# Kernel tuning notes

Hardware: AMD Instinct MI355X
Metric: run time of the kernel (lower is better)

## Reference

```python
import jax, jax.numpy as jnp
import numpy as np

N, DIM = 8192, 128

def setup_inputs() -> dict:
    key = jax.random.key(0)
    ks = jax.random.split(key, 9)
    s = 1.0 / np.sqrt(DIM)
    return {
        "x": jax.random.normal(ks[0], (N, DIM), dtype=jnp.float32),
        "Wq": jax.random.uniform(ks[1], (DIM, DIM), jnp.float32, -s, s),
        "bq": jax.random.uniform(ks[2], (DIM,), jnp.float32, -s, s),
        "Wk": jax.random.uniform(ks[3], (DIM, DIM), jnp.float32, -s, s),
        "bk": jax.random.uniform(ks[4], (DIM,), jnp.float32, -s, s),
        "Wv": jax.random.uniform(ks[5], (DIM, DIM), jnp.float32, -s, s),
        "bv": jax.random.uniform(ks[6], (DIM,), jnp.float32, -s, s),
        "Wo": jax.random.uniform(ks[7], (DIM, DIM), jnp.float32, -s, s),
        "bo": jax.random.uniform(ks[8], (DIM,), jnp.float32, -s, s),
    }

def reference(x, Wq, bq, Wk, bk, Wv, bv, Wo, bo):
    # nn.Linear: y = x @ W.T + b
    Q = x @ Wq.T + bq                      # [N, d]
    K = x @ Wk.T + bk                      # [N, d]
    V = x @ Wv.T + bv                      # [N, d]
    scale = 1.0 / jnp.sqrt(jnp.asarray(x.shape[-1], x.dtype))
    scores = (Q @ K.T) * scale             # [N, N] — matches original O(n^2) math
    attn = jax.nn.softmax(scores, axis=-1)
    out = attn @ V                         # [N, d]
    return out @ Wo.T + bo
```

## Files before the change

kernel.cpp:

```cpp
#include <hip/hip_runtime.h>
#include <math.h>


typedef __bf16 bf16x8 __attribute__((ext_vector_type(8)));
typedef float f32x4 __attribute__((ext_vector_type(4)));
typedef float f32x16 __attribute__((ext_vector_type(16)));
typedef unsigned int u32x4 __attribute__((ext_vector_type(4)));
typedef unsigned int u32x2 __attribute__((ext_vector_type(2)));
typedef unsigned short us16;

#define NTOK 8192
#define CHUNKS 8

static constexpr float SCALE_L2E = 0.08838834764831845f * 1.4426950408889634f;

__device__ __forceinline__ unsigned f2bf_u(float x) {
    unsigned u = __builtin_bit_cast(unsigned, x);
    return (u + 0x7FFFu + ((u >> 16) & 1u)) >> 16;
}

__device__ __forceinline__ unsigned pk_bf16(float x, float y) {
    unsigned a = __builtin_bit_cast(unsigned, x) + 0x8000u;
    unsigned b = __builtin_bit_cast(unsigned, y) + 0x8000u;
#if __has_builtin(__builtin_amdgcn_perm)
    return __builtin_amdgcn_perm(b, a, 0x07060302u);
#else
    return (a >> 16) | (b & 0xFFFF0000u);
#endif
}

__device__ __forceinline__ unsigned cvtpk_bf16(float x, float y) {
    unsigned r;
    asm("v_cvt_pk_bf16_f32 %0, %1, %2" : "=v"(r) : "v"(x), "v"(y));
    return r;
}

__device__ __forceinline__ void plswap(unsigned& a, unsigned& b) {
    asm("v_permlane32_swap_b32 %0, %1" : "+v"(a), "+v"(b));
}

__device__ __forceinline__ void pl16swap(unsigned& a, unsigned& b) {
    asm("v_permlane16_swap_b32 %0, %1" : "+v"(a), "+v"(b));
}

__device__ __forceinline__ float fexp2(float x) {
#if __has_builtin(__builtin_amdgcn_exp2f)
    return __builtin_amdgcn_exp2f(x);
#else
    return exp2f(x);
#endif
}

__device__ __forceinline__ bf16x8 ld_frag(const us16* p) {
    u32x4 u = *reinterpret_cast<const u32x4*>(p);
    return __builtin_bit_cast(bf16x8, u);
}

__device__ __forceinline__ bf16x8 cvt_frag(const float* p) {
    f32x4 a = *reinterpret_cast<const f32x4*>(p);
    f32x4 b = *reinterpret_cast<const f32x4*>(p + 4);
    u32x4 o;
    o[0] = f2bf_u(a[0]) | (f2bf_u(a[1]) << 16);
    o[1] = f2bf_u(a[2]) | (f2bf_u(a[3]) << 16);
    o[2] = f2bf_u(b[0]) | (f2bf_u(b[1]) << 16);
    o[3] = f2bf_u(b[2]) | (f2bf_u(b[3]) << 16);
    return __builtin_bit_cast(bf16x8, o);
}

__global__ __launch_bounds__(256) void proj_qkv(
    const float* __restrict__ x,
    const float* __restrict__ wq, const float* __restrict__ bq,
    const float* __restrict__ wk, const float* __restrict__ bk,
    const float* __restrict__ wv, const float* __restrict__ bv,
    us16* __restrict__ Qb, us16* __restrict__ Kb, us16* __restrict__ Vt)
{
    __shared__ us16 ldsT[4][16 * 136];

    int z = blockIdx.x >> 7;
    int tile = blockIdx.x & 127;
    const float* W = z == 0 ? wq : z == 1 ? wk : wv;
    const float* bias = z == 0 ? bq : z == 1 ? bk : bv;
    float osc = z == 0 ? SCALE_L2E : 1.0f;

    int w = threadIdx.x >> 6, lane = threadIdx.x & 63;
    int quad = lane >> 4, l15 = lane & 15;
    int rbase = tile * 64 + w * 16;

    bf16x8 af[4];
#pragma unroll
    for (int ks = 0; ks < 4; ++ks)
        af[ks] = cvt_frag(x + (rbase + l15) * 128 + ks * 32 + quad * 8);

    f32x4 acc[8];
#pragma unroll
    for (int nt = 0; nt < 8; ++nt) acc[nt] = f32x4{0.f, 0.f, 0.f, 0.f};

#pragma unroll
    for (int nt = 0; nt < 8; ++nt) {
#pragma unroll
        for (int ks = 0; ks < 4; ++ks) {
            bf16x8 bf = cvt_frag(W + (nt * 16 + l15) * 128 + ks * 32 + quad * 8);
            acc[nt] = __builtin_amdgcn_mfma_f32_16x16x32_bf16(af[ks], bf, acc[nt], 0, 0, 0);
        }
    }

    if (z < 2) {
        us16* T = &ldsT[w][0];
        us16* Out = z == 0 ? Qb : Kb;
#pragma unroll
        for (int nt = 0; nt < 8; ++nt) {
            float bb = bias[nt * 16 + l15];
#pragma unroll
            for (int r = 0; r < 4; ++r)
                T[(quad * 4 + r) * 136 + nt * 16 + l15] =
                    (us16)f2bf_u((acc[nt][r] + bb) * osc);
        }
        asm volatile("s_waitcnt lgkmcnt(0)" ::: "memory");
        __builtin_amdgcn_sched_barrier(0);
        int row = lane >> 2, seg = lane & 3;
        const us16* src = T + row * 136 + seg * 32;
        us16* dst = Out + (rbase + row) * 128 + seg * 32;
#pragma unroll
        for (int c = 0; c < 4; ++c)
            *reinterpret_cast<u32x4*>(dst + c * 8) =
                *reinterpret_cast<const u32x4*>(src + c * 8);
    } else {
#pragma unroll
        for (int nt = 0; nt < 8; ++nt) {
            float bb = bias[nt * 16 + l15];
            int d = nt * 16 + l15, r0 = rbase + quad * 4;
            u32x2 pk;
            pk[0] = f2bf_u(acc[nt][0] + bb) | (f2bf_u(acc[nt][1] + bb) << 16);
            pk[1] = f2bf_u(acc[nt][2] + bb) | (f2bf_u(acc[nt][3] + bb) << 16);
            *reinterpret_cast<u32x2*>(Vt + d * NTOK + r0) = pk;
        }
    }
}

__global__ __launch_bounds__(256, 2) void attn(
    const us16* __restrict__ Qb, const us16* __restrict__ Kb,
    const us16* __restrict__ Vt,
    float* __restrict__ Opart, float* __restrict__ Lpart)
{
    __shared__ us16 ldsK[2][64 * 136];
    __shared__ us16 ldsV[2][128 * 72];

    int qtile = blockIdx.x >> 3, chunk = blockIdx.x & 7;
    int tid = threadIdx.x, w = tid >> 6, lane = tid & 63;
    int quad = lane >> 4, l15 = lane & 15;
    int qb0 = qtile * 128 + w * 32;
    int k0 = chunk * 1024;

    bf16x8 qf[2][4];
#pragma unroll
    for (int mt = 0; mt < 2; ++mt)
#pragma unroll
        for (int ks = 0; ks < 4; ++ks)
            qf[mt][ks] = ld_frag(Qb + (qb0 + mt * 16 + l15) * 128 + ks * 32 + quad * 8);

    f32x4 o[2][8];
#pragma unroll
    for (int mt = 0; mt < 2; ++mt)
#pragma unroll
        for (int dt = 0; dt < 8; ++dt) o[mt][dt] = f32x4{0.f, 0.f, 0.f, 0.f};

    f32x4 lacc[2];
    lacc[0] = f32x4{0.f, 0.f, 0.f, 0.f};
    lacc[1] = f32x4{0.f, 0.f, 0.f, 0.f};

    u32x4 onesu;
    onesu[0] = onesu[1] = onesu[2] = onesu[3] = 0x3F803F80u;
    bf16x8 ones = __builtin_bit_cast(bf16x8, onesu);

#pragma unroll
    for (int c = 0; c < 4; ++c) {
        int idx = tid + c * 256, r = idx >> 4, cc = idx & 15;
        *reinterpret_cast<u32x4*>(&ldsK[0][0] + r * 136 + cc * 8) =
            *reinterpret_cast<const u32x4*>(Kb + (k0 + r) * 128 + cc * 8);
    }
#pragma unroll
    for (int c = 0; c < 4; ++c) {
        int idx = tid + c * 256, r = idx >> 3, cc = idx & 7;
        *reinterpret_cast<u32x4*>(&ldsV[0][0] + r * 72 + cc * 8) =
            *reinterpret_cast<const u32x4*>(Vt + (size_t)r * NTOK + k0 + cc * 8);
    }
    __syncthreads();

    for (int it = 0; it < 16; ++it) {
        int cur = it & 1;
        const us16* K_ = &ldsK[cur][0];
        const us16* V_ = &ldsV[cur][0];

        u32x4 kreg[4], vreg[4];
        if (it < 15) {
            int kk = k0 + (it + 1) * 64;
#pragma unroll
            for (int c = 0; c < 4; ++c) {
                int idx = tid + c * 256, r = idx >> 4, cc = idx & 15;
                kreg[c] = *reinterpret_cast<const u32x4*>(Kb + (kk + r) * 128 + cc * 8);
            }
#pragma unroll
            for (int c = 0; c < 4; ++c) {
                int idx = tid + c * 256, r = idx >> 3, cc = idx & 7;
                vreg[c] = *reinterpret_cast<const u32x4*>(Vt + (size_t)r * NTOK + kk + cc * 8);
            }
            __builtin_amdgcn_sched_barrier(0);
        }

        f32x4 s[2][4];
#pragma unroll
        for (int mt = 0; mt < 2; ++mt)
#pragma unroll
            for (int nt = 0; nt < 4; ++nt) s[mt][nt] = f32x4{0.f, 0.f, 0.f, 0.f};

        __builtin_amdgcn_s_setprio(1);
#pragma unroll
        for (int nt = 0; nt < 4; ++nt) {
#pragma unroll
            for (int ks = 0; ks < 4; ++ks) {
                bf16x8 kf = ld_frag(K_ + (nt * 16 + l15) * 136 + ks * 32 + quad * 8);
                s[0][nt] = __builtin_amdgcn_mfma_f32_16x16x32_bf16(kf, qf[0][ks], s[0][nt], 0, 0, 0);
                s[1][nt] = __builtin_amdgcn_mfma_f32_16x16x32_bf16(kf, qf[1][ks], s[1][nt], 0, 0, 0);
            }
        }
        __builtin_amdgcn_s_setprio(0);

        bf16x8 afP[2][2];
#pragma unroll
        for (int mt = 0; mt < 2; ++mt) {
            unsigned W[4][2];
#pragma unroll
            for (int nt = 0; nt < 4; ++nt) {
                float p0 = fexp2(s[mt][nt][0]);
                float p1 = fexp2(s[mt][nt][1]);
                float p2 = fexp2(s[mt][nt][2]);
                float p3 = fexp2(s[mt][nt][3]);
                W[nt][0] = cvtpk_bf16(p0, p1);
                W[nt][1] = cvtpk_bf16(p2, p3);
            }
#pragma unroll
            for (int k2 = 0; k2 < 2; ++k2) {
                u32x4 f;
                {
                    unsigned X = W[2 * k2][0], Y = W[2 * k2 + 1][0];
                    plswap(X, Y); pl16swap(X, Y);
                    f[0] = X; f[2] = Y;
                }
                {
                    unsigned X = W[2 * k2][1], Y = W[2 * k2 + 1][1];
                    plswap(X, Y); pl16swap(X, Y);
                    f[1] = X; f[3] = Y;
                }
                afP[mt][k2] = __builtin_bit_cast(bf16x8, f);
            }
        }

        lacc[0] = __builtin_amdgcn_mfma_f32_16x16x32_bf16(afP[0][0], ones, lacc[0], 0, 0, 0);
        lacc[0] = __builtin_amdgcn_mfma_f32_16x16x32_bf16(afP[0][1], ones, lacc[0], 0, 0, 0);
        lacc[1] = __builtin_amdgcn_mfma_f32_16x16x32_bf16(afP[1][0], ones, lacc[1], 0, 0, 0);
        lacc[1] = __builtin_amdgcn_mfma_f32_16x16x32_bf16(afP[1][1], ones, lacc[1], 0, 0, 0);

        __builtin_amdgcn_s_setprio(1);
#pragma unroll
        for (int dt = 0; dt < 8; ++dt) {
#pragma unroll
            for (int k2 = 0; k2 < 2; ++k2) {
                bf16x8 bv = ld_frag(V_ + (dt * 16 + l15) * 72 + k2 * 32 + quad * 8);
                o[0][dt] = __builtin_amdgcn_mfma_f32_16x16x32_bf16(afP[0][k2], bv, o[0][dt], 0, 0, 0);
                o[1][dt] = __builtin_amdgcn_mfma_f32_16x16x32_bf16(afP[1][k2], bv, o[1][dt], 0, 0, 0);
            }
        }
        __builtin_amdgcn_s_setprio(0);

        if (it < 15) {
            __builtin_amdgcn_sched_barrier(0);
#pragma unroll
            for (int c = 0; c < 4; ++c) {
                int idx = tid + c * 256, r = idx >> 4, cc = idx & 15;
                *reinterpret_cast<u32x4*>(&ldsK[cur ^ 1][0] + r * 136 + cc * 8) = kreg[c];
            }
#pragma unroll
            for (int c = 0; c < 4; ++c) {
                int idx = tid + c * 256, r = idx >> 3, cc = idx & 7;
                *reinterpret_cast<u32x4*>(&ldsV[cur ^ 1][0] + r * 72 + cc * 8) = vreg[c];
            }
        }
        __syncthreads();
    }

#pragma unroll
    for (int mt = 0; mt < 2; ++mt)
#pragma unroll
        for (int dt = 0; dt < 8; ++dt)
#pragma unroll
            for (int r = 0; r < 4; ++r) {
                int row = qb0 + mt * 16 + quad * 4 + r;
                Opart[(size_t)(chunk * NTOK + row) * 128 + dt * 16 + l15] = o[mt][dt][r];
            }
    if (l15 == 0) {
#pragma unroll
        for (int mt = 0; mt < 2; ++mt)
#pragma unroll
            for (int r = 0; r < 4; ++r) {
                int row = qb0 + mt * 16 + quad * 4 + r;
                Lpart[chunk * NTOK + row] = lacc[mt][r];
            }
    }
}

__global__ __launch_bounds__(256) void combine_proj(
    const float* __restrict__ Opart, const float* __restrict__ Lpart,
    const float* __restrict__ Wo, const float* __restrict__ bo,
    float* __restrict__ out)
{
    __shared__ us16 ldsO[32 * 136];
    __shared__ float ldsL[32];

    int tile = blockIdx.x, t = threadIdx.x;
    int r0 = tile * 32;

    if (t < 32) {
        float L = 0.f;
#pragma unroll
        for (int c = 0; c < CHUNKS; ++c) L += Lpart[c * NTOK + r0 + t];
        ldsL[t] = 1.0f / L;
    }

    f32x4 acc[4];
#pragma unroll
    for (int j = 0; j < 4; ++j) acc[j] = f32x4{0.f, 0.f, 0.f, 0.f};

#pragma unroll
    for (int c = 0; c < CHUNKS; ++c) {
        const float* src = Opart + (size_t)(c * NTOK + r0) * 128;
#pragma unroll
        for (int j = 0; j < 4; ++j) {
            f32x4 v = *reinterpret_cast<const f32x4*>(src + j * 1024 + t * 4);
            acc[j] += v;
        }
    }
    __syncthreads();

#pragma unroll
    for (int j = 0; j < 4; ++j) {
        int flat = j * 1024 + t * 4;
        int row = flat >> 7, col = flat & 127;
        float sc = ldsL[row];
        u32x2 wv;
        wv[0] = pk_bf16(acc[j][0] * sc, acc[j][1] * sc);
        wv[1] = pk_bf16(acc[j][2] * sc, acc[j][3] * sc);
        *reinterpret_cast<u32x2*>(ldsO + row * 136 + col) = wv;
    }
    __syncthreads();

    int w = t >> 6, lane = t & 63;
    int l31 = lane & 31, hi = lane >> 5;

    bf16x8 af[8];
#pragma unroll
    for (int ks = 0; ks < 8; ++ks)
        af[ks] = ld_frag(ldsO + l31 * 136 + ks * 16 + hi * 8);

    f32x16 acc2;
#pragma unroll
    for (int r = 0; r < 16; ++r) acc2[r] = 0.f;

#pragma unroll
    for (int ks = 0; ks < 8; ++ks) {
        bf16x8 bfw = cvt_frag(Wo + (w * 32 + l31) * 128 + ks * 16 + hi * 8);
        acc2 = __builtin_amdgcn_mfma_f32_32x32x16_bf16(af[ks], bfw, acc2, 0, 0, 0);
    }

    float bb = bo[w * 32 + l31];
#pragma unroll
    for (int r = 0; r < 16; ++r) {
        int m = (r & 3) + 8 * (r >> 2) + 4 * hi;
        out[(size_t)(r0 + m) * 128 + w * 32 + l31] = acc2[r] + bb;
    }
}

extern "C" void kernel_launch(void* const* d_in, const int* in_sizes, int n_in,
                              void* d_out, int out_size, void* d_ws, size_t ws_size,
                              hipStream_t stream)
{
    const float* x  = (const float*)d_in[0];
    const float* Wq = (const float*)d_in[1];
    const float* bq = (const float*)d_in[2];
    const float* Wk = (const float*)d_in[3];
    const float* bk = (const float*)d_in[4];
    const float* Wv = (const float*)d_in[5];
    const float* bv = (const float*)d_in[6];
    const float* Wo = (const float*)d_in[7];
    const float* bo = (const float*)d_in[8];

    char* ws = (char*)d_ws;
    const size_t MB = 1024 * 1024;
    us16* Qb  = (us16*)(ws + 0 * MB);
    us16* Kb  = (us16*)(ws + 2 * MB);
    us16* Vt  = (us16*)(ws + 4 * MB);
    float* Lp = (float*)(ws + 6 * MB);
    float* Op = (float*)(ws + 7 * MB);

    proj_qkv<<<384, 256, 0, stream>>>(x, Wq, bq, Wk, bk, Wv, bv, Qb, Kb, Vt);
    attn<<<512, 256, 0, stream>>>(Qb, Kb, Vt, Op, Lp);
    combine_proj<<<256, 256, 0, stream>>>(Op, Lp, Wo, bo, (float*)d_out);
}
```

Baseline: 139.6 us.

## Double attention block to 512 threads with 128-key tiles and shared K/V

The attention kernel now runs 8 waves per block covering 256 query rows, and 256 blocks instead of 512. Each loop iteration stages 128 keys instead of 64, processed in two halves, so half as many barriers and a larger K/V reuse across waves per LDS load. LDS grows to about 136 KB per block, which forces one block per CU and may reduce latency hiding; the grid also shrinks to 256 blocks, matching the CU count.

```diff
diff --git a/kernel.cpp b/kernel.cpp
--- a/kernel.cpp
+++ b/kernel.cpp
@@ -11,6 +11,8 @@
 
 #define NTOK 8192
 #define CHUNKS 8
+#define KT2 (128 * 136)
+#define VT2 (128 * 136)
 
 static constexpr float SCALE_L2E = 0.08838834764831845f * 1.4426950408889634f;
 
@@ -137,19 +139,22 @@
     }
 }
 
-__global__ __launch_bounds__(256, 2) void attn(
+__global__ __launch_bounds__(512, 1) void attn(
     const us16* __restrict__ Qb, const us16* __restrict__ Kb,
     const us16* __restrict__ Vt,
     float* __restrict__ Opart, float* __restrict__ Lpart)
 {
-    __shared__ us16 ldsK[2][64 * 136];
-    __shared__ us16 ldsV[2][128 * 72];
-
-    int qtile = blockIdx.x >> 3, chunk = blockIdx.x & 7;
+    __shared__ us16 smem[2 * KT2 + 2 * VT2];
+
+    int bid = blockIdx.x;
+    int qtile = bid >> 3, chunk = bid & 7;
     int tid = threadIdx.x, w = tid >> 6, lane = tid & 63;
     int quad = lane >> 4, l15 = lane & 15;
-    int qb0 = qtile * 128 + w * 32;
+    int qb0 = qtile * 256 + w * 32;
     int k0 = chunk * 1024;
+
+    us16* ldsK0 = smem;
+    us16* ldsV0 = smem + 2 * KT2;
 
     bf16x8 qf[2][4];
 #pragma unroll
@@ -174,115 +179,122 @@
 
 #pragma unroll
     for (int c = 0; c < 4; ++c) {
-        int idx = tid + c * 256, r = idx >> 4, cc = idx & 15;
-        *reinterpret_cast<u32x4*>(&ldsK[0][0] + r * 136 + cc * 8) =
+        int idx = tid + c * 512, r = idx >> 4, cc = idx & 15;
+        *reinterpret_cast<u32x4*>(ldsK0 + r * 136 + cc * 8) =
             *reinterpret_cast<const u32x4*>(Kb + (k0 + r) * 128 + cc * 8);
     }
 #pragma unroll
     for (int c = 0; c < 4; ++c) {
-        int idx = tid + c * 256, r = idx >> 3, cc = idx & 7;
-        *reinterpret_cast<u32x4*>(&ldsV[0][0] + r * 72 + cc * 8) =
+        int idx = tid + c * 512, r = idx >> 4, cc = idx & 15;
+        *reinterpret_cast<u32x4*>(ldsV0 + r * 136 + cc * 8) =
             *reinterpret_cast<const u32x4*>(Vt + (size_t)r * NTOK + k0 + cc * 8);
     }
     __syncthreads();
 
-    for (int it = 0; it < 16; ++it) {
+    for (int it = 0; it < 8; ++it) {
         int cur = it & 1;
-        const us16* K_ = &ldsK[cur][0];
-        const us16* V_ = &ldsV[cur][0];
+        const us16* K_ = ldsK0 + cur * KT2;
+        const us16* V_ = ldsV0 + cur * VT2;
 
         u32x4 kreg[4], vreg[4];
-        if (it < 15) {
-            int kk = k0 + (it + 1) * 64;
+        if (it < 7) {
+            int kk = k0 + (it + 1) * 128;
 #pragma unroll
             for (int c = 0; c < 4; ++c) {
-                int idx = tid + c * 256, r = idx >> 4, cc = idx & 15;
+                int idx = tid + c * 512, r = idx >> 4, cc = idx & 15;
                 kreg[c] = *reinterpret_cast<const u32x4*>(Kb + (kk + r) * 128 + cc * 8);
             }
 #pragma unroll
             for (int c = 0; c < 4; ++c) {
-                int idx = tid + c * 256, r = idx >> 3, cc = idx & 7;
+                int idx = tid + c * 512, r = idx >> 4, cc = idx & 15;
                 vreg[c] = *reinterpret_cast<const u32x4*>(Vt + (size_t)r * NTOK + kk + cc * 8);
             }
             __builtin_amdgcn_sched_barrier(0);
         }
 
-        f32x4 s[2][4];
-#pragma unroll
-        for (int mt = 0; mt < 2; ++mt)
-#pragma unroll
-            for (int nt = 0; nt < 4; ++nt) s[mt][nt] = f32x4{0.f, 0.f, 0.f, 0.f};
-
-        __builtin_amdgcn_s_setprio(1);
-#pragma unroll
-        for (int nt = 0; nt < 4; ++nt) {
-#pragma unroll
-            for (int ks = 0; ks < 4; ++ks) {
-                bf16x8 kf = ld_frag(K_ + (nt * 16 + l15) * 136 + ks * 32 + quad * 8);
-                s[0][nt] = __builtin_amdgcn_mfma_f32_16x16x32_bf16(kf, qf[0][ks], s[0][nt], 0, 0, 0);
-                s[1][nt] = __builtin_amdgcn_mfma_f32_16x16x32_bf16(kf, qf[1][ks], s[1][nt], 0, 0, 0);
-            }
-        }
-        __builtin_amdgcn_s_setprio(0);
-
-        bf16x8 afP[2][2];
-#pragma unroll
-        for (int mt = 0; mt < 2; ++mt) {
-            unsigned W[4][2];
+#pragma unroll
+        for (int half = 0; half < 2; ++half) {
+            int kb = half * 64;
+
+            f32x4 s[2][4];
+#pragma unroll
+            for (int mt = 0; mt < 2; ++mt)
+#pragma unroll
+                for (int nt = 0; nt < 4; ++nt) s[mt][nt] = f32x4{0.f, 0.f, 0.f, 0.f};
+
+            __builtin_amdgcn_s_setprio(1);
 #pragma unroll
             for (int nt = 0; nt < 4; ++nt) {
-                float p0 = fexp2(s[mt][nt][0]);
-                float p1 = fexp2(s[mt][nt][1]);
-                float p2 = fexp2(s[mt][nt][2]);
-                float p3 = fexp2(s[mt][nt][3]);
-                W[nt][0] = cvtpk_bf16(p0, p1);
-                W[nt][1] = cvtpk_bf16(p2, p3);
-            }
-#pragma unroll
-            for (int k2 = 0; k2 < 2; ++k2) {
-                u32x4 f;
-                {
-                    unsigned X = W[2 * k2][0], Y = W[2 * k2 + 1][0];
-                    plswap(X, Y); pl16swap(X, Y);
-                    f[0] = X; f[2] = Y;
+#pragma unroll
+                for (int ks = 0; ks < 4; ++ks) {
+                    bf16x8 kf = ld_frag(K_ + (kb + nt * 16 + l15) * 136 + ks * 32 + quad * 8);
+                    s[0][nt] = __builtin_amdgcn_mfma_f32_16x16x32_bf16(kf, qf[0][ks], s[0][nt], 0, 0, 0);
+                    s[1][nt] = __builtin_amdgcn_mfma_f32_16x16x32_bf16(kf, qf[1][ks], s[1][nt], 0, 0, 0);
                 }
-                {
-                    unsigned X = W[2 * k2][1], Y = W[2 * k2 + 1][1];
-                    plswap(X, Y); pl16swap(X, Y);
-                    f[1] = X; f[3] = Y;
+            }
+            __builtin_amdgcn_s_setprio(0);
+
+            bf16x8 afP[2][2];
+#pragma unroll
+            for (int mt = 0; mt < 2; ++mt) {
+                unsigned W[4][2];
+#pragma unroll
+                for (int nt = 0; nt < 4; ++nt) {
+                    float p0 = fexp2(s[mt][nt][0]);
+                    float p1 = fexp2(s[mt][nt][1]);
+                    float p2 = fexp2(s[mt][nt][2]);
+                    float p3 = fexp2(s[mt][nt][3]);
+                    W[nt][0] = cvtpk_bf16(p0, p1);
+                    W[nt][1] = cvtpk_bf16(p2, p3);
                 }
-                afP[mt][k2] = __builtin_bit_cast(bf16x8, f);
-            }
-        }
-
-        lacc[0] = __builtin_amdgcn_mfma_f32_16x16x32_bf16(afP[0][0], ones, lacc[0], 0, 0, 0);
-        lacc[0] = __builtin_amdgcn_mfma_f32_16x16x32_bf16(afP[0][1], ones, lacc[0], 0, 0, 0);
-        lacc[1] = __builtin_amdgcn_mfma_f32_16x16x32_bf16(afP[1][0], ones, lacc[1], 0, 0, 0);
-        lacc[1] = __builtin_amdgcn_mfma_f32_16x16x32_bf16(afP[1][1], ones, lacc[1], 0, 0, 0);
-
-        __builtin_amdgcn_s_setprio(1);
-#pragma unroll
-        for (int dt = 0; dt < 8; ++dt) {
-#pragma unroll
-            for (int k2 = 0; k2 < 2; ++k2) {
-                bf16x8 bv = ld_frag(V_ + (dt * 16 + l15) * 72 + k2 * 32 + quad * 8);
-                o[0][dt] = __builtin_amdgcn_mfma_f32_16x16x32_bf16(afP[0][k2], bv, o[0][dt], 0, 0, 0);
-                o[1][dt] = __builtin_amdgcn_mfma_f32_16x16x32_bf16(afP[1][k2], bv, o[1][dt], 0, 0, 0);
-            }
-        }
-        __builtin_amdgcn_s_setprio(0);
-
-        if (it < 15) {
+#pragma unroll
+                for (int k2 = 0; k2 < 2; ++k2) {
+                    u32x4 f;
+                    {
+                        unsigned X = W[2 * k2][0], Y = W[2 * k2 + 1][0];
+                        plswap(X, Y); pl16swap(X, Y);
+                        f[0] = X; f[2] = Y;
+                    }
+                    {
+                        unsigned X = W[2 * k2][1], Y = W[2 * k2 + 1][1];
+                        plswap(X, Y); pl16swap(X, Y);
+                        f[1] = X; f[3] = Y;
+                    }
+                    afP[mt][k2] = __builtin_bit_cast(bf16x8, f);
+                }
+            }
+
+            lacc[0] = __builtin_amdgcn_mfma_f32_16x16x32_bf16(afP[0][0], ones, lacc[0], 0, 0, 0);
+            lacc[0] = __builtin_amdgcn_mfma_f32_16x16x32_bf16(afP[0][1], ones, lacc[0], 0, 0, 0);
+            lacc[1] = __builtin_amdgcn_mfma_f32_16x16x32_bf16(afP[1][0], ones, lacc[1], 0, 0, 0);
+            lacc[1] = __builtin_amdgcn_mfma_f32_16x16x32_bf16(afP[1][1], ones, lacc[1], 0, 0, 0);
+
+            __builtin_amdgcn_s_setprio(1);
+#pragma unroll
+            for (int dt = 0; dt < 8; ++dt) {
+#pragma unroll
+                for (int k2 = 0; k2 < 2; ++k2) {
+                    bf16x8 bv = ld_frag(V_ + (dt * 16 + l15) * 136 + kb + k2 * 32 + quad * 8);
+                    o[0][dt] = __builtin_amdgcn_mfma_f32_16x16x32_bf16(afP[0][k2], bv, o[0][dt], 0, 0, 0);
+                    o[1][dt] = __builtin_amdgcn_mfma_f32_16x16x32_bf16(afP[1][k2], bv, o[1][dt], 0, 0, 0);
+                }
+            }
+            __builtin_amdgcn_s_setprio(0);
+        }
+
+        if (it < 7) {
             __builtin_amdgcn_sched_barrier(0);
+            us16* Kn = ldsK0 + (cur ^ 1) * KT2;
+            us16* Vn = ldsV0 + (cur ^ 1) * VT2;
 #pragma unroll
             for (int c = 0; c < 4; ++c) {
-                int idx = tid + c * 256, r = idx >> 4, cc = idx & 15;
-                *reinterpret_cast<u32x4*>(&ldsK[cur ^ 1][0] + r * 136 + cc * 8) = kreg[c];
+                int idx = tid + c * 512, r = idx >> 4, cc = idx & 15;
+                *reinterpret_cast<u32x4*>(Kn + r * 136 + cc * 8) = kreg[c];
             }
 #pragma unroll
             for (int c = 0; c < 4; ++c) {
-                int idx = tid + c * 256, r = idx >> 3, cc = idx & 7;
-                *reinterpret_cast<u32x4*>(&ldsV[cur ^ 1][0] + r * 72 + cc * 8) = vreg[c];
+                int idx = tid + c * 512, r = idx >> 4, cc = idx & 15;
+                *reinterpret_cast<u32x4*>(Vn + r * 136 + cc * 8) = vreg[c];
             }
         }
         __syncthreads();
@@ -402,6 +414,6 @@
     float* Op = (float*)(ws + 7 * MB);
 
     proj_qkv<<<384, 256, 0, stream>>>(x, Wq, bq, Wk, bk, Wv, bv, Qb, Kb, Vt);
-    attn<<<512, 256, 0, stream>>>(Qb, Kb, Vt, Op, Lp);
+    attn<<<256, 512, 0, stream>>>(Qb, Kb, Vt, Op, Lp);
     combine_proj<<<256, 256, 0, stream>>>(Op, Lp, Wo, bo, (float*)d_out);
 }
```

After: 138.0 us. No clear change (-1.2%).
